# Kernel tuning notes

Measured on AMD Instinct MI355X. Metric: run time of the kernel, lower is better.

## Reference

```python
import jax, jax.numpy as jnp
import numpy as np

N_HEADS = 16
HEAD = 64
HID = 1024
WIN = 256
LN_EPS = 1e-5


def _ln(x, g, b):
    m = jnp.mean(x, axis=-1, keepdims=True)
    v = jnp.mean((x - m) ** 2, axis=-1, keepdims=True)
    return (x - m) * jax.lax.rsqrt(v + LN_EPS) * g + b


def _window_shift(x):
    return jnp.concatenate([jnp.zeros_like(x[:, :WIN]), x[:, :-WIN]], axis=1)


def _additive_attn(x, vec, mask_add):
    B, S, _ = x.shape
    # per-head logits: (x * vec) summed within each head, scaled
    attn = (x * vec).reshape(B, S, N_HEADS, HEAD).sum(-1) / (HEAD ** 0.5)
    attn = jnp.exp(attn + mask_add)[..., None]          # [B,S,H,1]
    xh = x.reshape(B, S, N_HEADS, HEAD)
    s = jnp.cumsum(attn * xh, axis=1)
    s = s - _window_shift(s)                             # windowed cumsum of attn*x
    z = jnp.cumsum(attn, axis=1)
    z = z - _window_shift(z)                             # windowed cumsum of attn
    return (s / z).reshape(B, S, HID)


def setup_inputs():
    key = jax.random.key(0)
    ks = jax.random.split(key, 7)
    B, S = 4, 4096
    w = lambda k: (jax.random.normal(k, (HID, HID)) * 0.02).astype(jnp.float32)
    return {
        "hidden_states": jax.random.normal(ks[0], (B, S, HID), dtype=jnp.float32),
        "attention_mask": jnp.ones((B, S), dtype=jnp.float32),
        "Wq": w(ks[1]), "Wk": w(ks[2]), "Wv": w(ks[3]), "Wp": w(ks[4]),
        "query_attn": (jax.random.normal(ks[5], (HID,)) * 0.02).astype(jnp.float32),
        "key_attn": (jax.random.normal(ks[6], (HID,)) * 0.02).astype(jnp.float32),
        "ln1_g": jnp.ones((HID,), jnp.float32), "ln1_b": jnp.zeros((HID,), jnp.float32),
        "ln2_g": jnp.ones((HID,), jnp.float32), "ln2_b": jnp.zeros((HID,), jnp.float32),
    }


def reference(hidden_states, attention_mask, Wq, Wk, Wv, Wp, query_attn, key_attn,
              ln1_g, ln1_b, ln2_g, ln2_b):
    h = _ln(hidden_states, ln1_g, ln1_b)
    query = h @ Wq.T
    keys = h @ Wk.T
    values = h @ Wv.T
    mask_add = ((1.0 - attention_mask) * -10000.0)[:, :, None]  # [B,S,1]
    pooled_q = _additive_attn(query, query_attn, mask_add)
    pooled_q = pooled_q @ Wp.T                                  # (dropout is identity in eval)
    residual = h + pooled_q * keys
    mixed = _ln(residual, ln2_g, ln2_b)
    pooled_k = _additive_attn(mixed, key_attn, mask_add)
    return residual + pooled_k * values
```

## Files before the change

### kernel.cpp

```cpp
#include <hip/hip_runtime.h>
#include <hip/hip_bf16.h>

#define HID 1024
#define NH 16
#define HEAD 64
#define WIN 256
#define SEQ 4096
#define BATCH 4
#define NROWS (BATCH * SEQ)
#define LN_EPS 1e-5f

typedef unsigned short u16;
typedef __bf16 bf16x8 __attribute__((ext_vector_type(8)));
typedef float f32x4 __attribute__((ext_vector_type(4)));

static __device__ inline float bfu(u16 u) {
    union { unsigned int i; float f; } x;
    x.i = ((unsigned int)u) << 16;
    return x.f;
}

static __device__ inline u16 f2bf(float f) {
    union { float f; unsigned int i; } x;
    x.f = f;
    unsigned int lsb = (x.i >> 16) & 1u;
    x.i += 0x7fffu + lsb;
    return (u16)(x.i >> 16);
}

__global__ __launch_bounds__(256) void ln1_conv(
    const float* __restrict__ x, const float* __restrict__ g,
    const float* __restrict__ b, u16* __restrict__ out,
    const float* __restrict__ wq, const float* __restrict__ wk,
    const float* __restrict__ wv, const float* __restrict__ wp,
    u16* __restrict__ wo)
{
    __shared__ float red[8];
    int t = threadIdx.x;
    if (blockIdx.x >= NROWS) {
        int i = (blockIdx.x - NROWS) * 256 + t;
        const int n = 1024 * 1024;
        wo[i]         = f2bf(wq[i]);
        wo[n + i]     = f2bf(wk[i]);
        wo[2 * n + i] = f2bf(wv[i]);
        wo[3 * n + i] = f2bf(wp[i]);
        return;
    }
    int row = blockIdx.x;
    float4 v = ((const float4*)(x + (size_t)row * HID))[t];
    float s  = v.x + v.y + v.z + v.w;
    float ss = v.x * v.x + v.y * v.y + v.z * v.z + v.w * v.w;
    #pragma unroll
    for (int off = 32; off; off >>= 1) { s += __shfl_down(s, off); ss += __shfl_down(ss, off); }
    int wave = t >> 6, lane = t & 63;
    if (lane == 0) { red[wave] = s; red[4 + wave] = ss; }
    __syncthreads();
    float S  = red[0] + red[1] + red[2] + red[3];
    float SS = red[4] + red[5] + red[6] + red[7];
    float mean = S * (1.f / HID);
    float var  = SS * (1.f / HID) - mean * mean;
    float inv  = rsqrtf(var + LN_EPS);
    float4 gv = ((const float4*)g)[t];
    float4 bv = ((const float4*)b)[t];
    ushort4 o;
    o.x = f2bf((v.x - mean) * inv * gv.x + bv.x);
    o.y = f2bf((v.y - mean) * inv * gv.y + bv.y);
    o.z = f2bf((v.z - mean) * inv * gv.z + bv.z);
    o.w = f2bf((v.w - mean) * inv * gv.w + bv.w);
    ((ushort4*)(out + (size_t)row * HID))[t] = o;
}

#define GLDS(gp, lp) __builtin_amdgcn_global_load_lds( \
    (const __attribute__((address_space(1))) void*)(gp), \
    (__attribute__((address_space(3))) void*)(lp), 16, 0, 0)

__global__ __launch_bounds__(512, 4) void gemm_bk32(
    const u16* __restrict__ A, const u16* __restrict__ W,
    u16* __restrict__ C, int ldc)
{
    __shared__ __align__(16) u16 lds[3][12288];

    const int tid = threadIdx.x;
    const int wave = tid >> 6, lane = tid & 63;
    const int wr = wave >> 1, wc = wave & 1;
    const int li = lane & 15;
    const int kg = lane >> 4;
    const int swz = (kg * 8) ^ (((li >> 1) & 3) << 3);

    const int bm = (blockIdx.x & 7) * 8 + ((blockIdx.x >> 3) & 7);
    const int bn = blockIdx.x >> 6;

    const int rp = tid >> 2;
    const int colE = (((tid & 3) * 16) ^ (((rp >> 1) & 3) << 4)) >> 1;
    const int rowA0 = rp + (rp >= 64 ? 64 : 0);
    const u16* gA0 = A + (size_t)(bm * 256 + rowA0) * 1024 + colE;
    const u16* gA1 = gA0 + (size_t)64 * 1024;
    const u16* gB  = W + (size_t)(bn * 128 + rp) * 1024 + colE;

    const int aUnit = (wr & 1) * 4096;
    const int aRow0 = (wr >> 1) * 64;

    #pragma unroll
    for (int t = 0; t < 2; ++t) {
        u16* d = &lds[t][0];
        GLDS(gA0 + t * 32, d + tid * 8);
        GLDS(gA1 + t * 32, d + 4096 + tid * 8);
        GLDS(gB  + t * 32, d + 8192 + tid * 8);
    }
    asm volatile("s_waitcnt vmcnt(3)" ::: "memory");
    __builtin_amdgcn_sched_barrier(0);
    __builtin_amdgcn_s_barrier();
    __builtin_amdgcn_sched_barrier(0);

    f32x4 acc[4][4];
    #pragma unroll
    for (int m = 0; m < 4; ++m)
        #pragma unroll
        for (int n = 0; n < 4; ++n) {
            f32x4 z = {0.f, 0.f, 0.f, 0.f};
            acc[m][n] = z;
        }

    const u16* rb = &lds[0][0];
    const u16* rn = &lds[1][0];
    u16* wb = &lds[2][0];

    for (int kt = 0; kt < 32; ++kt) {
        bf16x8 bF[4], aF01[2];
        #pragma unroll
        for (int n = 0; n < 4; ++n)
            bF[n] = *(const bf16x8*)&rb[8192 + (wc * 64 + n * 16 + li) * 32 + swz];
        #pragma unroll
        for (int i = 0; i < 2; ++i)
            aF01[i] = *(const bf16x8*)&rb[aUnit + (aRow0 + i * 16 + li) * 32 + swz];

        if (kt < 30) {
            const int ko = (kt + 2) * 32;
            GLDS(gA0 + ko, wb + tid * 8);
            GLDS(gA1 + ko, wb + 4096 + tid * 8);
            GLDS(gB  + ko, wb + 8192 + tid * 8);
        }
        if (kt < 31) {
            if (kt < 30) asm volatile("s_waitcnt vmcnt(3)" ::: "memory");
            else         asm volatile("s_waitcnt vmcnt(0)" ::: "memory");
        }
        __builtin_amdgcn_sched_barrier(0);
        __builtin_amdgcn_s_barrier();
        __builtin_amdgcn_sched_barrier(0);

        __builtin_amdgcn_s_setprio(1);
        #pragma unroll
        for (int i = 0; i < 2; ++i)
            #pragma unroll
            for (int n = 0; n < 4; ++n)
                acc[i][n] = __builtin_amdgcn_mfma_f32_16x16x32_bf16(
                    aF01[i], bF[n], acc[i][n], 0, 0, 0);
        bf16x8 aF23[2];
        #pragma unroll
        for (int i = 0; i < 2; ++i)
            aF23[i] = *(const bf16x8*)&rb[aUnit + (aRow0 + (i + 2) * 16 + li) * 32 + swz];
        #pragma unroll
        for (int i = 0; i < 2; ++i)
            #pragma unroll
            for (int n = 0; n < 4; ++n)
                acc[2 + i][n] = __builtin_amdgcn_mfma_f32_16x16x32_bf16(
                    aF23[i], bF[n], acc[2 + i][n], 0, 0, 0);
        __builtin_amdgcn_s_setprio(0);
        __builtin_amdgcn_sched_barrier(0);
        __builtin_amdgcn_s_barrier();
        __builtin_amdgcn_sched_barrier(0);

        const u16* tmp = rb; rb = rn; rn = wb; wb = (u16*)tmp;
    }

    #pragma unroll
    for (int mf = 0; mf < 4; ++mf) {
        int row0 = bm * 256 + wr * 64 + mf * 16 + kg * 4;
        #pragma unroll
        for (int n = 0; n < 4; ++n) {
            int col = bn * 128 + wc * 64 + n * 16 + li;
            #pragma unroll
            for (int r = 0; r < 4; ++r)
                C[(size_t)(row0 + r) * ldc + col] = f2bf(acc[mf][n][r]);
        }
    }
}

__global__ __launch_bounds__(256) void logits_kernel(
    const u16* __restrict__ x, int xstride,
    const float* __restrict__ vec, const float* __restrict__ mask,
    float* __restrict__ aw)
{
    int h = blockIdx.y, b = blockIdx.z;
    int s = blockIdx.x * 256 + threadIdx.x;
    __shared__ float vl[HEAD];
    if (threadIdx.x < HEAD) vl[threadIdx.x] = vec[h * HEAD + threadIdx.x];
    __syncthreads();
    const uint4* xr = (const uint4*)(x + ((size_t)(b * SEQ + s)) * xstride + h * HEAD);
    float dot = 0.f;
    #pragma unroll
    for (int i = 0; i < 8; ++i) {
        uint4 v = xr[i];
        const u16* p = (const u16*)&v;
        #pragma unroll
        for (int j = 0; j < 8; ++j) dot += bfu(p[j]) * vl[i * 8 + j];
    }
    float ma = (1.0f - mask[b * SEQ + s]) * -10000.0f;
    aw[((size_t)b * NH + h) * SEQ + s] = expf(dot * 0.125f + ma);
}

__global__ __launch_bounds__(512) void attn_win2(
    const u16* __restrict__ x, int xstride,
    const float* __restrict__ aw_g,
    u16* __restrict__ out_bf,
    const u16* __restrict__ resv,
    float* __restrict__ outF,
    int fused)
{
    int c = blockIdx.x, h2 = blockIdx.y, b = blockIdx.z;
    __shared__ float awl[2][2][WIN];
    __shared__ float2 sts[2][8][64];
    __shared__ float stz[2][8][2];

    int t = threadIdx.x, wave = t >> 6, lane = t & 63;
    int hh = lane >> 5;
    int coff = hh * 64 + (lane & 31) * 2;
    bool havePrev = (c > 0);

    const float* aw0 = aw_g + ((size_t)b * NH + h2 * 2) * SEQ;
    for (int i = t; i < 1024; i += 512) {
        int hd = i >> 9, cc = (i >> 8) & 1, j = i & 255;
        float v = 0.f;
        if (cc == 1) v = aw0[hd * SEQ + c * WIN + j];
        else if (havePrev) v = aw0[hd * SEQ + (c - 1) * WIN + j];
        awl[hd][cc][j] = v;
    }
    __syncthreads();

    const u16* xb = x + (size_t)b * SEQ * xstride + h2 * 128 + coff;
    int jp0 = (havePrev ? c - 1 : c) * WIN;
    int jc0 = c * WIN;
    int j0 = wave * 32;

    float s0a = 0, s0b = 0, s1a = 0, s1b = 0, z0 = 0, z1 = 0;
    #pragma unroll 8
    for (int jj = 0; jj < 32; ++jj) {
        int j = j0 + jj;
        float ap = awl[hh][0][j], ac = awl[hh][1][j];
        unsigned up = *(const unsigned*)(xb + (size_t)(jp0 + j) * xstride);
        unsigned uc = *(const unsigned*)(xb + (size_t)(jc0 + j) * xstride);
        s0a += ap * bfu(up & 0xffff); s0b += ap * bfu(up >> 16); z0 += ap;
        s1a += ac * bfu(uc & 0xffff); s1b += ac * bfu(uc >> 16); z1 += ac;
    }
    sts[0][wave][lane] = make_float2(s0a, s0b);
    sts[1][wave][lane] = make_float2(s1a, s1b);
    if ((lane & 31) == 0) { stz[0][wave][hh] = z0; stz[1][wave][hh] = z1; }
    __syncthreads();

    float cs0a = 0, cs0b = 0, cs1a = 0, cs1b = 0, cz0 = 0, cz1 = 0;
    float totsa = 0, totsb = 0, totz = 0;
    #pragma unroll
    for (int w2 = 0; w2 < 8; ++w2) {
        float2 sp = sts[0][w2][lane];
        float zp = stz[0][w2][hh];
        totsa += sp.x; totsb += sp.y; totz += zp;
        if (w2 < wave) {
            cs0a += sp.x; cs0b += sp.y; cz0 += zp;
            float2 sc = sts[1][w2][lane];
            cs1a += sc.x; cs1b += sc.y; cz1 += stz[1][w2][hh];
        }
    }

    float rpa = cs0a, rpb = cs0b, rca = cs1a, rcb = cs1b, rzp = cz0, rzc = cz1;
    size_t rowbase = (size_t)b * SEQ + jc0;
    #pragma unroll 4
    for (int jj = 0; jj < 32; ++jj) {
        int j = j0 + jj;
        float ap = awl[hh][0][j], ac = awl[hh][1][j];
        unsigned up = *(const unsigned*)(xb + (size_t)(jp0 + j) * xstride);
        unsigned uc = *(const unsigned*)(xb + (size_t)(jc0 + j) * xstride);
        rpa += ap * bfu(up & 0xffff); rpb += ap * bfu(up >> 16); rzp += ap;
        rca += ac * bfu(uc & 0xffff); rcb += ac * bfu(uc >> 16); rzc += ac;
        float inv = 1.f / (rzc + totz - rzp);
        float wva = (rca + totsa - rpa) * inv;
        float wvb = (rcb + totsb - rpb) * inv;
        if (fused) {
            size_t roff = (rowbase + j) * 3072 + h2 * 128 + coff;
            unsigned rr = *(const unsigned*)(resv + roff);
            unsigned vv = *(const unsigned*)(resv + roff + 2048);
            float2 o;
            o.x = bfu(rr & 0xffff) + wva * bfu(vv & 0xffff);
            o.y = bfu(rr >> 16)    + wvb * bfu(vv >> 16);
            *(float2*)(outF + (rowbase + j) * HID + h2 * 128 + coff) = o;
        } else {
            unsigned pk = (unsigned)f2bf(wva) | ((unsigned)f2bf(wvb) << 16);
            *(unsigned*)(out_bf + (rowbase + j) * HID + h2 * 128 + coff) = pk;
        }
    }
}

__global__ __launch_bounds__(256) void resid_ln2(
    const u16* h, u16* qkv,
    const float* __restrict__ g, const float* __restrict__ b,
    const float* __restrict__ ka, const float* __restrict__ mask,
    u16* mixed, float* __restrict__ aw2)
{
    int row = blockIdx.x;
    int t = threadIdx.x;
    ushort4 h4 = ((const ushort4*)(h + (size_t)row * HID))[t];
    ushort4 p4 = ((const ushort4*)(qkv + (size_t)row * 3072))[t];
    ushort4 k4 = ((const ushort4*)(qkv + (size_t)row * 3072 + 1024))[t];
    float r0 = bfu(h4.x) + bfu(p4.x) * bfu(k4.x);
    float r1 = bfu(h4.y) + bfu(p4.y) * bfu(k4.y);
    float r2 = bfu(h4.z) + bfu(p4.z) * bfu(k4.z);
    float r3 = bfu(h4.w) + bfu(p4.w) * bfu(k4.w);
    ushort4 rb;
    rb.x = f2bf(r0); rb.y = f2bf(r1); rb.z = f2bf(r2); rb.w = f2bf(r3);
    ((ushort4*)(qkv + (size_t)row * 3072))[t] = rb;

    float s  = r0 + r1 + r2 + r3;
    float ss = r0 * r0 + r1 * r1 + r2 * r2 + r3 * r3;
    __shared__ float red[8];
    #pragma unroll
    for (int off = 32; off; off >>= 1) { s += __shfl_down(s, off); ss += __shfl_down(ss, off); }
    int wave = t >> 6, lane = t & 63;
    if (lane == 0) { red[wave] = s; red[4 + wave] = ss; }
    __syncthreads();
    float S  = red[0] + red[1] + red[2] + red[3];
    float SS = red[4] + red[5] + red[6] + red[7];
    float mean = S * (1.f / HID);
    float var  = SS * (1.f / HID) - mean * mean;
    float inv  = rsqrtf(var + LN_EPS);
    float4 gv = ((const float4*)g)[t];
    float4 bv = ((const float4*)b)[t];
    float n0 = (r0 - mean) * inv * gv.x + bv.x;
    float n1 = (r1 - mean) * inv * gv.y + bv.y;
    float n2 = (r2 - mean) * inv * gv.z + bv.z;
    float n3 = (r3 - mean) * inv * gv.w + bv.w;
    ushort4 o;
    o.x = f2bf(n0); o.y = f2bf(n1); o.z = f2bf(n2); o.w = f2bf(n3);
    ((ushort4*)(mixed + (size_t)row * HID))[t] = o;

    float4 kv = ((const float4*)ka)[t];
    float partial = n0 * kv.x + n1 * kv.y + n2 * kv.z + n3 * kv.w;
    partial += __shfl_xor(partial, 1);
    partial += __shfl_xor(partial, 2);
    partial += __shfl_xor(partial, 4);
    partial += __shfl_xor(partial, 8);
    if ((t & 15) == 0) {
        int hh = t >> 4;
        int bb = row >> 12, sl = row & (SEQ - 1);
        float ma = (1.0f - mask[row]) * -10000.0f;
        aw2[((size_t)bb * NH + hh) * SEQ + sl] = expf(partial * 0.125f + ma);
    }
}

extern "C" void kernel_launch(void* const* d_in, const int* in_sizes, int n_in,
                              void* d_out, int out_size, void* d_ws, size_t ws_size,
                              hipStream_t stream)
{
    const float* hidden = (const float*)d_in[0];
    const float* mask   = (const float*)d_in[1];
    const float* Wq     = (const float*)d_in[2];
    const float* Wk     = (const float*)d_in[3];
    const float* Wv     = (const float*)d_in[4];
    const float* Wp     = (const float*)d_in[5];
    const float* qa     = (const float*)d_in[6];
    const float* ka     = (const float*)d_in[7];
    const float* g1     = (const float*)d_in[8];
    const float* b1     = (const float*)d_in[9];
    const float* g2     = (const float*)d_in[10];
    const float* b2     = (const float*)d_in[11];
    float* out = (float*)d_out;

    char* ws = (char*)d_ws;
    u16* wbf = (u16*)ws;       ws += (size_t)4 * 1024 * 1024 * 2;
    u16* hbf = (u16*)ws;       ws += (size_t)NROWS * HID * 2;
    u16* qkv = (u16*)ws;       ws += (size_t)NROWS * 3072 * 2;
    u16* pooled = (u16*)ws;    ws += (size_t)NROWS * HID * 2;
    float* aw1 = (float*)ws;   ws += (size_t)BATCH * NH * SEQ * 4;
    float* aw2 = (float*)ws;

    ln1_conv<<<NROWS + 4096, 256, 0, stream>>>(hidden, g1, b1, hbf, Wq, Wk, Wv, Wp, wbf);
    gemm_bk32<<<1536, 512, 0, stream>>>(hbf, wbf, qkv, 3072);
    logits_kernel<<<dim3(SEQ / 256, NH, BATCH), 256, 0, stream>>>(qkv, 3072, qa, mask, aw1);
    attn_win2<<<dim3(SEQ / WIN, NH / 2, BATCH), 512, 0, stream>>>(
        qkv, 3072, aw1, pooled, (const u16*)nullptr, (float*)nullptr, 0);
    gemm_bk32<<<512, 512, 0, stream>>>(pooled, wbf + (size_t)3 * 1024 * 1024, qkv, 3072);
    resid_ln2<<<NROWS, 256, 0, stream>>>(hbf, qkv, g2, b2, ka, mask, hbf, aw2);
    attn_win2<<<dim3(SEQ / WIN, NH / 2, BATCH), 512, 0, stream>>>(
        hbf, HID, aw2, (u16*)nullptr, qkv, out, 1);
}
```

Measured before the change: 288.2 us.

## Fuse query attention logits into QKV GEMM epilogue and remap tile order

The separate logits kernel is removed. Its per-head dot product with query_attn, the mask add and the exp are now computed in the QKV GEMM epilogue from the fp32 accumulators, reduced with lane shuffles. The block-to-tile mapping also changes so that consecutive blocks walk across the N tiles of a row band, which alters L2 reuse of A and W. This saves one kernel launch and a re-read of the query columns, at the cost of extra epilogue work. The logits now come from unrounded fp32 values instead of the bf16 values stored in qkv.

```diff
diff --git a/kernel.cpp b/kernel.cpp
--- a/kernel.cpp
+++ b/kernel.cpp
@@ -76,7 +76,10 @@
 
 __global__ __launch_bounds__(512, 4) void gemm_bk32(
     const u16* __restrict__ A, const u16* __restrict__ W,
-    u16* __restrict__ C, int ldc)
+    u16* __restrict__ C, int ldc, int nbn,
+    const float* __restrict__ qa,
+    const float* __restrict__ mask,
+    float* __restrict__ awout)
 {
     __shared__ __align__(16) u16 lds[3][12288];
 
@@ -87,8 +90,9 @@
     const int kg = lane >> 4;
     const int swz = (kg * 8) ^ (((li >> 1) & 3) << 3);
 
-    const int bm = (blockIdx.x & 7) * 8 + ((blockIdx.x >> 3) & 7);
-    const int bn = blockIdx.x >> 6;
+    const int local = blockIdx.x >> 3;
+    const int bn = local % nbn;
+    const int bm = (blockIdx.x & 7) * 8 + local / nbn;
 
     const int rp = tid >> 2;
     const int colE = (((tid & 3) * 16) ^ (((rp >> 1) & 3) << 4)) >> 1;
@@ -173,6 +177,31 @@
         const u16* tmp = rb; rb = rn; rn = wb; wb = (u16*)tmp;
     }
 
+    if (awout != nullptr && bn < 8) {
+        float qav[4];
+        #pragma unroll
+        for (int n = 0; n < 4; ++n)
+            qav[n] = qa[bn * 128 + wc * 64 + n * 16 + li];
+        #pragma unroll
+        for (int mf = 0; mf < 4; ++mf) {
+            #pragma unroll
+            for (int r = 0; r < 4; ++r) {
+                float d = acc[mf][0][r] * qav[0] + acc[mf][1][r] * qav[1]
+                        + acc[mf][2][r] * qav[2] + acc[mf][3][r] * qav[3];
+                d += __shfl_xor(d, 1);
+                d += __shfl_xor(d, 2);
+                d += __shfl_xor(d, 4);
+                d += __shfl_xor(d, 8);
+                if (li == 0) {
+                    int row = bm * 256 + wr * 64 + mf * 16 + kg * 4 + r;
+                    float ma = (1.0f - mask[row]) * -10000.0f;
+                    awout[(((size_t)(row >> 12)) * NH + bn * 2 + wc) * SEQ + (row & (SEQ - 1))] =
+                        expf(d * 0.125f + ma);
+                }
+            }
+        }
+    }
+
     #pragma unroll
     for (int mf = 0; mf < 4; ++mf) {
         int row0 = bm * 256 + wr * 64 + mf * 16 + kg * 4;
@@ -184,29 +213,6 @@
                 C[(size_t)(row0 + r) * ldc + col] = f2bf(acc[mf][n][r]);
         }
     }
-}
-
-__global__ __launch_bounds__(256) void logits_kernel(
-    const u16* __restrict__ x, int xstride,
-    const float* __restrict__ vec, const float* __restrict__ mask,
-    float* __restrict__ aw)
-{
-    int h = blockIdx.y, b = blockIdx.z;
-    int s = blockIdx.x * 256 + threadIdx.x;
-    __shared__ float vl[HEAD];
-    if (threadIdx.x < HEAD) vl[threadIdx.x] = vec[h * HEAD + threadIdx.x];
-    __syncthreads();
-    const uint4* xr = (const uint4*)(x + ((size_t)(b * SEQ + s)) * xstride + h * HEAD);
-    float dot = 0.f;
-    #pragma unroll
-    for (int i = 0; i < 8; ++i) {
-        uint4 v = xr[i];
-        const u16* p = (const u16*)&v;
-        #pragma unroll
-        for (int j = 0; j < 8; ++j) dot += bfu(p[j]) * vl[i * 8 + j];
-    }
-    float ma = (1.0f - mask[b * SEQ + s]) * -10000.0f;
-    aw[((size_t)b * NH + h) * SEQ + s] = expf(dot * 0.125f + ma);
 }
 
 __global__ __launch_bounds__(512) void attn_win2(
@@ -382,11 +388,11 @@
     float* aw2 = (float*)ws;
 
     ln1_conv<<<NROWS + 4096, 256, 0, stream>>>(hidden, g1, b1, hbf, Wq, Wk, Wv, Wp, wbf);
-    gemm_bk32<<<1536, 512, 0, stream>>>(hbf, wbf, qkv, 3072);
-    logits_kernel<<<dim3(SEQ / 256, NH, BATCH), 256, 0, stream>>>(qkv, 3072, qa, mask, aw1);
+    gemm_bk32<<<1536, 512, 0, stream>>>(hbf, wbf, qkv, 3072, 24, qa, mask, aw1);
     attn_win2<<<dim3(SEQ / WIN, NH / 2, BATCH), 512, 0, stream>>>(
         qkv, 3072, aw1, pooled, (const u16*)nullptr, (float*)nullptr, 0);
-    gemm_bk32<<<512, 512, 0, stream>>>(pooled, wbf + (size_t)3 * 1024 * 1024, qkv, 3072);
+    gemm_bk32<<<512, 512, 0, stream>>>(pooled, wbf + (size_t)3 * 1024 * 1024, qkv, 3072, 8,
+                                       (const float*)nullptr, (const float*)nullptr, (float*)nullptr);
     resid_ln2<<<NROWS, 256, 0, stream>>>(hbf, qkv, g2, b2, ka, mask, hbf, aw2);
     attn_win2<<<dim3(SEQ / WIN, NH / 2, BATCH), 512, 0, stream>>>(
         hbf, HID, aw2, (u16*)nullptr, qkv, out, 1);
```

Result: slower. 294.3 us (+2.1%).
